# Performance work log

Measured on AMD Instinct MI355X. Metric: run time of the kernel, lower is better.

## Reference

```python
import jax, jax.numpy as jnp
import numpy as np

EPS = 1e-5  # BatchNorm1d eps


def _glorot(key, shape):
    fan_in, fan_out = shape[0], shape[1]
    lim = float(np.sqrt(6.0 / (fan_in + fan_out)))
    return jax.random.uniform(key, shape, jnp.float32, -lim, lim)


def setup_inputs() -> dict:
    key = jax.random.key(0)
    ks = jax.random.split(key, 6)
    N, IN, H, OUT = 50000, 128, 64, 64
    E = 800000
    x = jax.random.normal(ks[0], (N, IN), jnp.float32)
    edge_index = jax.random.randint(ks[1], (2, E), 0, N, jnp.int64)
    return {
        "x": x,
        "edge_index": edge_index,
        "W1": _glorot(ks[2], (IN, H)),
        "b1": jnp.zeros((H,), jnp.float32),
        "gamma1": jnp.ones((H,), jnp.float32),
        "beta1": jnp.zeros((H,), jnp.float32),
        "W2": _glorot(ks[3], (H, OUT)),
        "b2": jnp.zeros((OUT,), jnp.float32),
        "gamma2": jnp.ones((OUT,), jnp.float32),
        "beta2": jnp.zeros((OUT,), jnp.float32),
    }


def _gcn_conv(x, W, b, src, dst, norm, n):
    # x' = D^{-1/2} (A + I) D^{-1/2} X W + b  (PyG GCNConv, edge_weight=None)
    h = x @ W                              # [N, F]
    msg = h[src] * norm[:, None]           # gather + scale, [E+N, F]
    out = jax.ops.segment_sum(msg, dst, num_segments=n)  # scatter-add
    return out + b


def _batch_norm(h, gamma, beta):
    # training-mode BN over node dim, biased variance (as torch uses for normalization)
    mean = h.mean(0)
    var = h.var(0)
    return (h - mean) * jax.lax.rsqrt(var + EPS) * gamma + beta


def reference(x, edge_index, W1, b1, gamma1, beta1, W2, b2, gamma2, beta2):
    n = x.shape[0]
    # add self loops
    loop = jnp.arange(n, dtype=edge_index.dtype)
    src = jnp.concatenate([edge_index[0], loop])
    dst = jnp.concatenate([edge_index[1], loop])
    # symmetric degree normalization (deg >= 1 thanks to self loops)
    deg = jax.ops.segment_sum(jnp.ones(src.shape[0], x.dtype), dst, num_segments=n)
    dinv = jax.lax.rsqrt(jnp.maximum(deg, 1e-12))
    norm = dinv[src] * dinv[dst]           # [E+N]

    # layer 1: GCNConv -> BN -> ReLU (dropout = identity in eval)
    h = _gcn_conv(x, W1, b1, src, dst, norm, n)
    h = jax.nn.relu(_batch_norm(h, gamma1, beta1))
    # layer 2: GCNConv -> BN (no activation on last layer)
    h = _gcn_conv(h, W2, b2, src, dst, norm, n)
    h = _batch_norm(h, gamma2, beta2)
    return h
```

## Files before the change

### kernel.cpp

```cpp
#include <hip/hip_runtime.h>
#include <hip/hip_fp16.h>
#include <math.h>

#define EPS 1e-5f
#define CAP 64

typedef float v4f __attribute__((ext_vector_type(4)));

__global__ void k_init(int* __restrict__ cnt, float* __restrict__ stats,
                       __half* __restrict__ Ylo, __half* __restrict__ Yhi,
                       unsigned short* __restrict__ csr, int N) {
    int i = blockIdx.x * blockDim.x + threadIdx.x;
    if (i < N) {
        cnt[i] = 0;
        int4* p = (int4*)(csr + (size_t)i * CAP);
#pragma unroll
        for (int k = 0; k < 8; ++k) p[k] = make_int4(-1, -1, -1, -1);
    }
    if (i < 256) stats[i] = 0.0f;
    if (i < 16) {
        ((int*)(Ylo + (size_t)N * 32))[i] = 0;
        ((int*)(Yhi + (size_t)N * 32))[i] = 0;
    }
}

__global__ void k_dinv(const int* __restrict__ cnt, float* __restrict__ dinv, int N) {
    int i = blockIdx.x * blockDim.x + threadIdx.x;
    if (i < N) dinv[i] = rsqrtf((float)(cnt[i] + 1));
    if (i == 0) dinv[N] = 0.0f;
}

__global__ __launch_bounds__(256) void k_gemm1_fill(const float* __restrict__ x,
                                                    const float* __restrict__ W1,
                                                    __half* __restrict__ Ylo,
                                                    __half* __restrict__ Yhi, int N,
                                                    const int* __restrict__ src,
                                                    const int* __restrict__ dst,
                                                    int* __restrict__ cnt,
                                                    unsigned short* __restrict__ csr,
                                                    int E, int G) {
    if ((int)blockIdx.x >= G) {
        int t = (blockIdx.x - G) * 256 + threadIdx.x;
        int stride = (gridDim.x - G) * 256;
        for (int e = t; e < E; e += stride) {
            int d = dst[e];
            int pos = atomicAdd(&cnt[d], 1);
            if (pos < CAP)
                __builtin_nontemporal_store((unsigned short)src[e], &csr[(size_t)d * CAP + pos]);
        }
        return;
    }
    __shared__ float w[128 * 64];
    __shared__ float xs[4][4][128];
    for (int i = threadIdx.x; i < 128 * 64; i += 256) w[i] = W1[i];
    __syncthreads();
    int lane = threadIdx.x & 63;
    int wave = threadIdx.x >> 6;
    int half = lane >> 5, l = lane & 31;
    __half* Yout = half ? Yhi : Ylo;
    int gwave = blockIdx.x * 4 + wave;
    int nw = G * 4;
    for (int r0 = gwave * 4; r0 < N; r0 += nw * 4) {
        int nr = min(4, N - r0);
        for (int j = 0; j < nr; ++j) {
            xs[wave][j][lane]      = x[(size_t)(r0 + j) * 128 + lane];
            xs[wave][j][64 + lane] = x[(size_t)(r0 + j) * 128 + 64 + lane];
        }
        float a0 = 0.f, a1 = 0.f, a2 = 0.f, a3 = 0.f;
#pragma unroll 8
        for (int k = 0; k < 128; ++k) {
            float wk = w[k * 64 + lane];
            a0 += xs[wave][0][k] * wk;
            a1 += xs[wave][1][k] * wk;
            a2 += xs[wave][2][k] * wk;
            a3 += xs[wave][3][k] * wk;
        }
        Yout[(size_t)(r0 + 0) * 32 + l] = __float2half(a0);
        if (nr > 1) Yout[(size_t)(r0 + 1) * 32 + l] = __float2half(a1);
        if (nr > 2) Yout[(size_t)(r0 + 2) * 32 + l] = __float2half(a2);
        if (nr > 3) Yout[(size_t)(r0 + 3) * 32 + l] = __float2half(a3);
    }
}

template <bool PRESCALED>
__global__ __launch_bounds__(256) void k_agg(const __half* __restrict__ Ylo,
                                             const __half* __restrict__ Yhi,
                                             const unsigned short* __restrict__ csr,
                                             const int* __restrict__ cnt,
                                             const float* __restrict__ dinv,
                                             float* __restrict__ H,
                                             float* __restrict__ stats, int N) {
    __shared__ float ssum[4][32], ssq[4][32];
    int half = blockIdx.x & 1;
    const __half* Y = half ? Yhi : Ylo;
    int lane = threadIdx.x & 63;
    int wave = threadIdx.x >> 6;
    int g = lane >> 3;
    int fl = lane & 7;
    int slot = (blockIdx.x >> 1) * 4 + wave;
    int nslots = (gridDim.x >> 1) * 4;
    float s0 = 0.f, s1 = 0.f, s2 = 0.f, s3 = 0.f;
    float q0 = 0.f, q1 = 0.f, q2 = 0.f, q3 = 0.f;
    union U8 { double d; __half2 h[2]; };
    for (int v = slot; v < N; v += nslots) {
        int c = min(cnt[v], CAP);
        float dv = dinv[v];
        int ent = (int)csr[(size_t)v * CAP + lane];
        float a0, a1, a2, a3;
        {
            U8 u; u.d = *(const double*)(Y + (size_t)v * 32 + fl * 4);
            float2 p0 = __half22float2(u.h[0]);
            float2 p1 = __half22float2(u.h[1]);
            float selfw = (g == 0) ? (PRESCALED ? 1.f : dv) : 0.f;
            a0 = selfw * p0.x; a1 = selfw * p0.y;
            a2 = selfw * p1.x; a3 = selfw * p1.y;
        }
        int nb = (c + 7) >> 3;
        for (int b = 0; b < nb; ++b) {
            int idx = __shfl(ent, b * 8 + g, 64);
            idx = min(idx, N);
            float de = PRESCALED ? 1.f : dinv[idx];
            U8 u; u.d = *(const double*)(Y + (size_t)idx * 32 + fl * 4);
            float2 p0 = __half22float2(u.h[0]);
            float2 p1 = __half22float2(u.h[1]);
            a0 += de * p0.x; a1 += de * p0.y;
            a2 += de * p1.x; a3 += de * p1.y;
        }
#pragma unroll
        for (int m = 8; m <= 32; m <<= 1) {
            a0 += __shfl_xor(a0, m, 64);
            a1 += __shfl_xor(a1, m, 64);
            a2 += __shfl_xor(a2, m, 64);
            a3 += __shfl_xor(a3, m, 64);
        }
        if (g == 0) {
            a0 *= dv; a1 *= dv; a2 *= dv; a3 *= dv;
            v4f hv = {a0, a1, a2, a3};
            __builtin_nontemporal_store(hv, (v4f*)(H + (size_t)v * 64 + half * 32 + fl * 4));
            s0 += a0; s1 += a1; s2 += a2; s3 += a3;
            q0 += a0 * a0; q1 += a1 * a1; q2 += a2 * a2; q3 += a3 * a3;
        }
    }
    if (g == 0) {
        ssum[wave][4 * fl + 0] = s0; ssum[wave][4 * fl + 1] = s1;
        ssum[wave][4 * fl + 2] = s2; ssum[wave][4 * fl + 3] = s3;
        ssq[wave][4 * fl + 0] = q0;  ssq[wave][4 * fl + 1] = q1;
        ssq[wave][4 * fl + 2] = q2;  ssq[wave][4 * fl + 3] = q3;
    }
    __syncthreads();
    if (threadIdx.x < 32) {
        float ts = ssum[0][threadIdx.x] + ssum[1][threadIdx.x] + ssum[2][threadIdx.x] + ssum[3][threadIdx.x];
        float tq = ssq[0][threadIdx.x] + ssq[1][threadIdx.x] + ssq[2][threadIdx.x] + ssq[3][threadIdx.x];
        atomicAdd(&stats[half * 32 + threadIdx.x], ts);
        atomicAdd(&stats[64 + half * 32 + threadIdx.x], tq);
    }
}

__global__ __launch_bounds__(256) void k_gemm2(const float* __restrict__ H1,
                                               const float* __restrict__ stats,
                                               const float* __restrict__ gamma,
                                               const float* __restrict__ beta,
                                               const float* __restrict__ W2,
                                               const float* __restrict__ dinv,
                                               __half* __restrict__ Ylo,
                                               __half* __restrict__ Yhi, int N) {
    __shared__ float w[64 * 64];
    __shared__ float xs[4][4][64];
    for (int i = threadIdx.x; i < 64 * 64; i += 256) w[i] = W2[i];
    int lane = threadIdx.x & 63;
    int wave = threadIdx.x >> 6;
    int half = lane >> 5, l = lane & 31;
    __half* Yout = half ? Yhi : Ylo;
    float mean = stats[lane] / (float)N;
    float var = stats[64 + lane] / (float)N - mean * mean;
    float rstd = rsqrtf(var + EPS);
    float g = gamma[lane], bt = beta[lane];
    __syncthreads();
    int gwave = blockIdx.x * 4 + wave;
    int nw = gridDim.x * 4;
    for (int r0 = gwave * 4; r0 < N; r0 += nw * 4) {
        int nr = min(4, N - r0);
        for (int j = 0; j < nr; ++j) {
            float v = H1[(size_t)(r0 + j) * 64 + lane];
            v = (v - mean) * rstd * g + bt;
            xs[wave][j][lane] = fmaxf(v, 0.f);
        }
        float a0 = 0.f, a1 = 0.f, a2 = 0.f, a3 = 0.f;
#pragma unroll 8
        for (int k = 0; k < 64; ++k) {
            float wk = w[k * 64 + lane];
            a0 += xs[wave][0][k] * wk;
            a1 += xs[wave][1][k] * wk;
            a2 += xs[wave][2][k] * wk;
            a3 += xs[wave][3][k] * wk;
        }
        Yout[(size_t)(r0 + 0) * 32 + l] = __float2half(a0 * dinv[r0]);
        if (nr > 1) Yout[(size_t)(r0 + 1) * 32 + l] = __float2half(a1 * dinv[r0 + 1]);
        if (nr > 2) Yout[(size_t)(r0 + 2) * 32 + l] = __float2half(a2 * dinv[r0 + 2]);
        if (nr > 3) Yout[(size_t)(r0 + 3) * 32 + l] = __float2half(a3 * dinv[r0 + 3]);
    }
}

__global__ void k_bnfinal(float* __restrict__ out, const float* __restrict__ stats,
                          const float* __restrict__ gamma, const float* __restrict__ beta,
                          int N) {
    int i = blockIdx.x * blockDim.x + threadIdx.x;
    int total = N * 64;
    if (i < total) {
        int f = i & 63;
        float mean = stats[f] / (float)N;
        float var = stats[64 + f] / (float)N - mean * mean;
        float rstd = rsqrtf(var + EPS);
        out[i] = (out[i] - mean) * rstd * gamma[f] + beta[f];
    }
}

extern "C" void kernel_launch(void* const* d_in, const int* in_sizes, int n_in,
                              void* d_out, int out_size, void* d_ws, size_t ws_size,
                              hipStream_t stream) {
    const float* x      = (const float*)d_in[0];
    const int*   ei     = (const int*)d_in[1];
    const float* W1     = (const float*)d_in[2];
    const float* gamma1 = (const float*)d_in[4];
    const float* beta1  = (const float*)d_in[5];
    const float* W2     = (const float*)d_in[6];
    const float* gamma2 = (const float*)d_in[8];
    const float* beta2  = (const float*)d_in[9];
    float* out = (float*)d_out;

    const int N = in_sizes[0] / 128;
    const int E = in_sizes[1] / 2;
    const int* src = ei;
    const int* dst = ei + E;

    char* ws = (char*)d_ws;
    int*   cnt   = (int*)  ws;
    float* stats = (float*)(ws + 0x40000);
    float* dinv  = (float*)(ws + 0x50000);
    __half* Ylo  = (__half*)(ws + 0x90000);
    __half* Yhi  = (__half*)(ws + 0x90000 + 0x320000);
    float* H1    = (float*)(ws + 0x90000 + 0x640000);
    unsigned short* csr = (unsigned short*)(ws + 0x90000 + 0x640000 + 0xC40000);

    const int B = (N + 255) / 256;
    const int total = N * 64;
    const int G = 768, F = 256;

    k_init<<<B, 256, 0, stream>>>(cnt, stats, Ylo, Yhi, csr, N);

    k_gemm1_fill<<<G + F, 256, 0, stream>>>(x, W1, Ylo, Yhi, N, src, dst, cnt, csr, E, G);
    k_dinv<<<B, 256, 0, stream>>>(cnt, dinv, N);
    k_agg<false><<<2048, 256, 0, stream>>>(Ylo, Yhi, csr, cnt, dinv, H1, stats, N);

    k_gemm2<<<1024, 256, 0, stream>>>(H1, stats, gamma1, beta1, W2, dinv, Ylo, Yhi, N);
    k_agg<true><<<2048, 256, 0, stream>>>(Ylo, Yhi, csr, cnt, dinv, out, stats + 128, N);
    k_bnfinal<<<(total + 255) / 256, 256, 0, stream>>>(out, stats + 128, gamma2, beta2, N);
}
```

Measured before the change: 267.1 us.

## Process four nodes per wave in aggregation with two edge halves each

Restructures the aggregation kernel so each wave handles four destination nodes at once. Each node gets 16 lanes, split into two halves that read packed pairs of CSR entries, instead of one node per wave processed in 8-neighbour batches. The cross-group shuffle reduction per node shrinks to a single xor-32 step, and BN statistics are reduced once at the end. This aims to cut the lanes left idle on low-degree nodes and the per-node shuffle overhead, at the cost of divergence when degrees differ among the four nodes. The grid is resized to 1250 blocks to match.

```diff
diff --git a/kernel.cpp b/kernel.cpp
--- a/kernel.cpp
+++ b/kernel.cpp
@@ -6,6 +6,10 @@
 #define CAP 64
 
 typedef float v4f __attribute__((ext_vector_type(4)));
+
+__device__ __forceinline__ float xor32sum(float a) {
+    return a + __shfl_xor(a, 32, 64);
+}
 
 __global__ void k_init(int* __restrict__ cnt, float* __restrict__ stats,
                        __half* __restrict__ Ylo, __half* __restrict__ Yhi,
@@ -95,30 +99,37 @@
     const __half* Y = half ? Yhi : Ylo;
     int lane = threadIdx.x & 63;
     int wave = threadIdx.x >> 6;
-    int g = lane >> 3;
     int fl = lane & 7;
+    int node = (lane >> 3) & 3;
+    int gsh = (lane >> 5) << 4;
+    float selfmask = (lane < 32) ? 1.f : 0.f;
     int slot = (blockIdx.x >> 1) * 4 + wave;
     int nslots = (gridDim.x >> 1) * 4;
     float s0 = 0.f, s1 = 0.f, s2 = 0.f, s3 = 0.f;
     float q0 = 0.f, q1 = 0.f, q2 = 0.f, q3 = 0.f;
     union U8 { double d; __half2 h[2]; };
-    for (int v = slot; v < N; v += nslots) {
-        int c = min(cnt[v], CAP);
-        float dv = dinv[v];
-        int ent = (int)csr[(size_t)v * CAP + lane];
+    for (int base = slot * 4; base < N; base += nslots * 4) {
+        int myv = base + node;
+        bool vok = myv < N;
+        int vs = vok ? myv : N;
+        int c  = vok ? min(cnt[myv], CAP) : 0;
+        float dv = dinv[vs];
+        const unsigned int* crow =
+            (const unsigned int*)(csr + (size_t)(vok ? myv : 0) * CAP);
         float a0, a1, a2, a3;
         {
-            U8 u; u.d = *(const double*)(Y + (size_t)v * 32 + fl * 4);
+            U8 u; u.d = *(const double*)(Y + (size_t)vs * 32 + fl * 4);
             float2 p0 = __half22float2(u.h[0]);
             float2 p1 = __half22float2(u.h[1]);
-            float selfw = (g == 0) ? (PRESCALED ? 1.f : dv) : 0.f;
+            float selfw = selfmask * (PRESCALED ? 1.f : dv);
             a0 = selfw * p0.x; a1 = selfw * p0.y;
             a2 = selfw * p1.x; a3 = selfw * p1.y;
         }
-        int nb = (c + 7) >> 3;
-        for (int b = 0; b < nb; ++b) {
-            int idx = __shfl(ent, b * 8 + g, 64);
-            idx = min(idx, N);
+        for (int b = 0; b < 32; ++b) {
+            if (__all(2 * b >= c)) break;
+            unsigned int w = crow[b];
+            int ent = vok ? (int)((w >> gsh) & 0xFFFFu) : 0xFFFF;
+            int idx = min(ent, N);
             float de = PRESCALED ? 1.f : dinv[idx];
             U8 u; u.d = *(const double*)(Y + (size_t)idx * 32 + fl * 4);
             float2 p0 = __half22float2(u.h[0]);
@@ -126,22 +137,25 @@
             a0 += de * p0.x; a1 += de * p0.y;
             a2 += de * p1.x; a3 += de * p1.y;
         }
+        a0 = xor32sum(a0) * dv;
+        a1 = xor32sum(a1) * dv;
+        a2 = xor32sum(a2) * dv;
+        a3 = xor32sum(a3) * dv;
+        if (lane < 32 && vok) {
+            v4f hv = {a0, a1, a2, a3};
+            __builtin_nontemporal_store(hv, (v4f*)(H + (size_t)myv * 64 + half * 32 + fl * 4));
+        }
+        s0 += a0; s1 += a1; s2 += a2; s3 += a3;
+        q0 += a0 * a0; q1 += a1 * a1; q2 += a2 * a2; q3 += a3 * a3;
+    }
 #pragma unroll
-        for (int m = 8; m <= 32; m <<= 1) {
-            a0 += __shfl_xor(a0, m, 64);
-            a1 += __shfl_xor(a1, m, 64);
-            a2 += __shfl_xor(a2, m, 64);
-            a3 += __shfl_xor(a3, m, 64);
-        }
-        if (g == 0) {
-            a0 *= dv; a1 *= dv; a2 *= dv; a3 *= dv;
-            v4f hv = {a0, a1, a2, a3};
-            __builtin_nontemporal_store(hv, (v4f*)(H + (size_t)v * 64 + half * 32 + fl * 4));
-            s0 += a0; s1 += a1; s2 += a2; s3 += a3;
-            q0 += a0 * a0; q1 += a1 * a1; q2 += a2 * a2; q3 += a3 * a3;
-        }
-    }
-    if (g == 0) {
+    for (int m = 8; m <= 16; m <<= 1) {
+        s0 += __shfl_xor(s0, m, 64); s1 += __shfl_xor(s1, m, 64);
+        s2 += __shfl_xor(s2, m, 64); s3 += __shfl_xor(s3, m, 64);
+        q0 += __shfl_xor(q0, m, 64); q1 += __shfl_xor(q1, m, 64);
+        q2 += __shfl_xor(q2, m, 64); q3 += __shfl_xor(q3, m, 64);
+    }
+    if (lane < 8) {
         ssum[wave][4 * fl + 0] = s0; ssum[wave][4 * fl + 1] = s1;
         ssum[wave][4 * fl + 2] = s2; ssum[wave][4 * fl + 3] = s3;
         ssq[wave][4 * fl + 0] = q0;  ssq[wave][4 * fl + 1] = q1;
@@ -250,9 +264,9 @@
 
     k_gemm1_fill<<<G + F, 256, 0, stream>>>(x, W1, Ylo, Yhi, N, src, dst, cnt, csr, E, G);
     k_dinv<<<B, 256, 0, stream>>>(cnt, dinv, N);
-    k_agg<false><<<2048, 256, 0, stream>>>(Ylo, Yhi, csr, cnt, dinv, H1, stats, N);
+    k_agg<false><<<1250, 256, 0, stream>>>(Ylo, Yhi, csr, cnt, dinv, H1, stats, N);
 
     k_gemm2<<<1024, 256, 0, stream>>>(H1, stats, gamma1, beta1, W2, dinv, Ylo, Yhi, N);
-    k_agg<true><<<2048, 256, 0, stream>>>(Ylo, Yhi, csr, cnt, dinv, out, stats + 128, N);
+    k_agg<true><<<1250, 256, 0, stream>>>(Ylo, Yhi, csr, cnt, dinv, out, stats + 128, N);
     k_bnfinal<<<(total + 255) / 256, 256, 0, stream>>>(out, stats + 128, gamma2, beta2, N);
 }
```

Result: no change. 265.3 us (-0.7%).
